# Optimization experiments

Measured on AMD Instinct MI355X. Metric: run time of the kernel, lower is better.

## Reference

```python
import jax, jax.numpy as jnp
import numpy as np

B, S, DIM, HEADS, FFN = 2, 2048, 2048, 16, 8192
HD = DIM // HEADS            # 128
F_, H_, W_ = 8, 16, 16       # F*H*W == S (video token grid)
CTX = 512
EPS = 1e-6


def _rope_tables(max_len=1024):
    # Wan-style rope_params: per-axis inverse-frequency tables, concatenated columns [22|21|21].
    c = HD // 2  # 64 complex channels
    splits = [c - 2 * (c // 3), c // 3, c // 3]
    pos = np.arange(max_len)[:, None].astype(np.float64)
    parts = []
    for d in splits:
        inv = 1.0 / (10000.0 ** (np.arange(d, dtype=np.float64) / d))
        parts.append(pos * inv[None, :])
    theta = np.concatenate(parts, axis=1)  # [max_len, 64]
    return (jnp.asarray(np.cos(theta), jnp.float32),
            jnp.asarray(np.sin(theta), jnp.float32))


def setup_inputs() -> dict:
    key = jax.random.key(0)
    ks = iter(jax.random.split(key, 40))
    def nrm(shape, scale=1.0):
        return jax.random.normal(next(ks), shape, jnp.float32) * scale
    ws = DIM ** -0.5
    cos, sin = _rope_tables()
    inp = dict(
        x=nrm((B, S, DIM)),
        e=nrm((B, 6, DIM)),
        context=nrm((B, CTX, DIM)),
        freqs_cos=cos, freqs_sin=sin,
        modulation=nrm((1, 6, DIM), ws),
        # self-attention (weights stored [in, out] so y = x @ W + b)
        sa_wq=nrm((DIM, DIM), ws), sa_bq=jnp.zeros((DIM,), jnp.float32),
        sa_wk=nrm((DIM, DIM), ws), sa_bk=jnp.zeros((DIM,), jnp.float32),
        sa_wv=nrm((DIM, DIM), ws), sa_bv=jnp.zeros((DIM,), jnp.float32),
        sa_wo=nrm((DIM, DIM), ws), sa_bo=jnp.zeros((DIM,), jnp.float32),
        sa_nq=jnp.ones((DIM,), jnp.float32), sa_nk=jnp.ones((DIM,), jnp.float32),
        # t2v cross-attention
        ca_wq=nrm((DIM, DIM), ws), ca_bq=jnp.zeros((DIM,), jnp.float32),
        ca_wk=nrm((DIM, DIM), ws), ca_bk=jnp.zeros((DIM,), jnp.float32),
        ca_wv=nrm((DIM, DIM), ws), ca_bv=jnp.zeros((DIM,), jnp.float32),
        ca_wo=nrm((DIM, DIM), ws), ca_bo=jnp.zeros((DIM,), jnp.float32),
        ca_nq=jnp.ones((DIM,), jnp.float32), ca_nk=jnp.ones((DIM,), jnp.float32),
        norm3_w=jnp.ones((DIM,), jnp.float32), norm3_b=jnp.zeros((DIM,), jnp.float32),
        ffn_w1=nrm((DIM, FFN), ws), ffn_b1=jnp.zeros((FFN,), jnp.float32),
        ffn_w2=nrm((FFN, DIM), FFN ** -0.5), ffn_b2=jnp.zeros((DIM,), jnp.float32),
    )
    return inp


def _ln(x, w=None, b=None, eps=EPS):
    m = jnp.mean(x, -1, keepdims=True)
    v = jnp.mean((x - m) ** 2, -1, keepdims=True)
    y = (x - m) * jax.lax.rsqrt(v + eps)
    return y * w + b if w is not None else y


def _rms(x, w, eps=EPS):
    return x * jax.lax.rsqrt(jnp.mean(x * x, -1, keepdims=True) + eps) * w


def _grid_cs(tab):
    # tab: [1024, 64] -> per-token table [S, 64] for grid (F_,H_,W_), split 22/21/21
    c = HD // 2
    s0 = c - 2 * (c // 3)  # 22
    s1 = c // 3            # 21
    f = jnp.broadcast_to(tab[:F_, :s0][:, None, None, :], (F_, H_, W_, s0))
    h = jnp.broadcast_to(tab[:H_, s0:s0 + s1][None, :, None, :], (F_, H_, W_, s1))
    w = jnp.broadcast_to(tab[:W_, s0 + s1:][None, None, :, :], (F_, H_, W_, s1))
    return jnp.concatenate([f, h, w], -1).reshape(S, c)


def _rope(x, cos, sin):
    # x: [B,S,N,D]; complex rotation on consecutive (even, odd) pairs
    xp = x.reshape(*x.shape[:-1], HD // 2, 2)
    xr, xi = xp[..., 0], xp[..., 1]
    c = cos[None, :, None, :]
    s = sin[None, :, None, :]
    return jnp.stack([xr * c - xi * s, xr * s + xi * c], -1).reshape(x.shape)


def _attn(q, k, v):
    logits = jnp.einsum('bqnd,bknd->bnqk', q, k) / np.float32(np.sqrt(HD))
    w = jax.nn.softmax(logits, axis=-1)
    return jnp.einsum('bnqk,bknd->bqnd', w, v)


def reference(x, e, context, freqs_cos, freqs_sin, modulation,
              sa_wq, sa_bq, sa_wk, sa_bk, sa_wv, sa_bv, sa_wo, sa_bo, sa_nq, sa_nk,
              ca_wq, ca_bq, ca_wk, ca_bk, ca_wv, ca_bv, ca_wo, ca_bo, ca_nq, ca_nk,
              norm3_w, norm3_b, ffn_w1, ffn_b1, ffn_w2, ffn_b2,
              seq_lens=None, grid_sizes=None, context_lens=None):
    # AdaLN modulation: 6 (shift, scale, gate) vectors per sample
    em = modulation + e                       # [B,6,D]
    e0, e1, e2, e3, e4, e5 = [em[:, i:i + 1, :] for i in range(6)]
    cos = _grid_cs(freqs_cos)
    sin = _grid_cs(freqs_sin)

    # --- self-attention with modulated LayerNorm + 3D RoPE ---
    xn = _ln(x) * (1 + e1) + e0
    q = _rms(xn @ sa_wq + sa_bq, sa_nq).reshape(B, S, HEADS, HD)
    k = _rms(xn @ sa_wk + sa_bk, sa_nk).reshape(B, S, HEADS, HD)
    v = (xn @ sa_wv + sa_bv).reshape(B, S, HEADS, HD)
    y = _attn(_rope(q, cos, sin), _rope(k, cos, sin), v).reshape(B, S, DIM)
    x = x + (y @ sa_wo + sa_bo) * e2

    # --- t2v cross-attention (affine norm3) ---
    xn3 = _ln(x, norm3_w, norm3_b)
    q = _rms(xn3 @ ca_wq + ca_bq, ca_nq).reshape(B, S, HEADS, HD)
    k = _rms(context @ ca_wk + ca_bk, ca_nk).reshape(B, CTX, HEADS, HD)
    v = (context @ ca_wv + ca_bv).reshape(B, CTX, HEADS, HD)
    y = _attn(q, k, v).reshape(B, S, DIM)
    x = x + (y @ ca_wo + ca_bo)

    # --- modulated FFN (GELU-tanh) ---
    xn2 = _ln(x) * (1 + e4) + e3
    y = jax.nn.gelu(xn2 @ ffn_w1 + ffn_b1, approximate=True) @ ffn_w2 + ffn_b2
    return x + y * e5
```

## Files before the change

### kernel.cpp

```cpp
#include <hip/hip_runtime.h>
#include <hip/hip_bf16.h>
#include <math.h>

#define DIMX 2048
#define SLEN 2048
#define BSZ 2
#define NHEADS 16
#define HDIM 128
#define FFND 8192
#define CTXL 512
#define LN_EPS 1e-6f

typedef __attribute__((ext_vector_type(8))) short short8_t;
typedef __attribute__((ext_vector_type(4))) short short4_t;
typedef __attribute__((ext_vector_type(4))) float f32x4;
typedef __hip_bfloat16 bf16;

__device__ __forceinline__ short f2bf(float f) {
  union { float f; unsigned u; } v; v.f = f;
  return (short)((v.u + 0x7FFFu + ((v.u >> 16) & 1u)) >> 16);
}
__device__ __forceinline__ float bf2f(short s) {
  union { unsigned u; float f; } v; v.u = ((unsigned)(unsigned short)s) << 16;
  return v.f;
}

__device__ __forceinline__ void gload16(const void* g, void* l) {
  __builtin_amdgcn_global_load_lds(
      (const __attribute__((address_space(1))) unsigned int*)g,
      (__attribute__((address_space(3))) unsigned int*)l, 16, 0, 0);
}

__device__ __forceinline__ float wred_sum(float v) {
#pragma unroll
  for (int o = 32; o > 0; o >>= 1) v += __shfl_xor(v, o, 64);
  return v;
}

__global__ void em_kernel(const float* __restrict__ e, const float* __restrict__ mod,
                          float* __restrict__ em, int n) {
  int i = blockIdx.x * 256 + threadIdx.x;
  if (i < n) em[i] = e[i] + mod[i % (6 * DIMX)];
}

__global__ void cvt_kernel(const float* __restrict__ in, bf16* __restrict__ out, int n8) {
  int i = blockIdx.x * 256 + threadIdx.x;
  if (i >= n8) return;
  float4 a = *(const float4*)(in + (size_t)i * 8);
  float4 b = *(const float4*)(in + (size_t)i * 8 + 4);
  float fv[8] = {a.x, a.y, a.z, a.w, b.x, b.y, b.z, b.w};
  short8_t o;
#pragma unroll
  for (int j = 0; j < 8; ++j) o[j] = f2bf(fv[j]);
  *(short8_t*)((short*)out + (size_t)i * 8) = o;
}

__global__ void packb_kernel(const float* b0, const float* b1, const float* b2,
                             float* __restrict__ dst, int n) {
  int i = blockIdx.x * 256 + threadIdx.x;
  if (i >= n) return;
  int seg = i >> 11, j = i & 2047;
  const float* s = seg == 0 ? b0 : (seg == 1 ? b1 : b2);
  dst[i] = s[j];
}

__global__ __launch_bounds__(256) void transpose_w(const float* __restrict__ W,
                                                   bf16* __restrict__ Wt, int K, int N,
                                                   int noff) {
  __shared__ short tile[64 * 68];
  int k0 = blockIdx.y << 6, n0 = blockIdx.x << 6;
  int t = threadIdx.x;
#pragma unroll
  for (int p = 0; p < 4; ++p) {
    int lin = p * 1024 + t * 4;
    int kr = lin >> 6, nc = lin & 63;
    float4 f = *(const float4*)(W + (size_t)(k0 + kr) * N + n0 + nc);
    tile[(nc + 0) * 68 + kr] = f2bf(f.x);
    tile[(nc + 1) * 68 + kr] = f2bf(f.y);
    tile[(nc + 2) * 68 + kr] = f2bf(f.z);
    tile[(nc + 3) * 68 + kr] = f2bf(f.w);
  }
  __syncthreads();
#pragma unroll
  for (int p = 0; p < 4; ++p) {
    int lin = p * 1024 + t * 4;
    int nr = lin >> 6, kc = lin & 63;
    short4_t s = *(const short4_t*)&tile[nr * 68 + kc];
    *(short4_t*)((short*)Wt + (size_t)(noff + n0 + nr) * K + k0 + kc) = s;
  }
}

__global__ __launch_bounds__(256) void ln_kernel(
    const float* __restrict__ x, const float* __restrict__ gamma,
    const float* __restrict__ beta, int gbstride, float addone,
    int rows_per_b, bf16* __restrict__ out) {
  int row = blockIdx.x;
  int t = threadIdx.x;
  const float* xr = x + (size_t)row * DIMX;
  float4 v0 = *(const float4*)(xr + t * 8);
  float4 v1 = *(const float4*)(xr + t * 8 + 4);
  float vv[8] = {v0.x, v0.y, v0.z, v0.w, v1.x, v1.y, v1.z, v1.w};
  float s = 0.f, ss = 0.f;
#pragma unroll
  for (int i = 0; i < 8; ++i) { s += vv[i]; ss += vv[i] * vv[i]; }
  __shared__ float red[8];
  s = wred_sum(s); ss = wred_sum(ss);
  int wid = t >> 6;
  if ((t & 63) == 0) { red[wid] = s; red[4 + wid] = ss; }
  __syncthreads();
  float sum = red[0] + red[1] + red[2] + red[3];
  float sumsq = red[4] + red[5] + red[6] + red[7];
  float mean = sum * (1.f / DIMX);
  float var = sumsq * (1.f / DIMX) - mean * mean;
  float rs = rsqrtf(var + LN_EPS);
  int b = row / rows_per_b;
  const float* g = gamma + (size_t)b * gbstride;
  const float* be = beta + (size_t)b * gbstride;
  short8_t o;
#pragma unroll
  for (int i = 0; i < 8; ++i) {
    int d = t * 8 + i;
    float y = (vv[i] - mean) * rs;
    o[i] = f2bf(y * (addone + g[d]) + be[d]);
  }
  *(short8_t*)((short*)out + (size_t)row * DIMX + t * 8) = o;
}

__global__ __launch_bounds__(256) void rms_rope_kernel(
    const bf16* __restrict__ x, int xstride, const float* __restrict__ w,
    const float* __restrict__ fcos, const float* __restrict__ fsin,
    int do_rope, bf16* __restrict__ out) {
  int row = blockIdx.x;
  int t = threadIdx.x;
  short8_t xi = *(const short8_t*)((const short*)x + (size_t)row * xstride + t * 8);
  float vv[8];
#pragma unroll
  for (int i = 0; i < 8; ++i) vv[i] = bf2f(xi[i]);
  float ss = 0.f;
#pragma unroll
  for (int i = 0; i < 8; ++i) ss += vv[i] * vv[i];
  __shared__ float red[4];
  ss = wred_sum(ss);
  int wid = t >> 6;
  if ((t & 63) == 0) red[wid] = ss;
  __syncthreads();
  float sumsq = red[0] + red[1] + red[2] + red[3];
  float rs = rsqrtf(sumsq * (1.f / DIMX) + LN_EPS);
  float y[8];
#pragma unroll
  for (int i = 0; i < 8; ++i) y[i] = vv[i] * rs * w[t * 8 + i];
  if (do_rope) {
    int s = row % SLEN;
    int f = s >> 8, hh = (s >> 4) & 15, ww = s & 15;
    int jb = ((t * 8) % HDIM) >> 1;
#pragma unroll
    for (int p = 0; p < 4; ++p) {
      int j = jb + p;
      int src = (j < 22) ? f : ((j < 43) ? hh : ww);
      float c = fcos[src * 64 + j];
      float sn = fsin[src * 64 + j];
      float xr_ = y[2 * p], xim = y[2 * p + 1];
      y[2 * p] = xr_ * c - xim * sn;
      y[2 * p + 1] = xr_ * sn + xim * c;
    }
  }
  short8_t o;
#pragma unroll
  for (int i = 0; i < 8; ++i) o[i] = f2bf(y[i]);
  *(short8_t*)((short*)out + (size_t)row * DIMX + t * 8) = o;
}

__global__ __launch_bounds__(256) void gemm_bt(
    const bf16* __restrict__ A, const bf16* __restrict__ Bt,
    const float* __restrict__ bias,
    float* outF, bf16* outB,
    const float* resid, const float* __restrict__ scale,
    int scstride, int rows_per_b, int gn, int N, int K, int mode) {
  __shared__ short As[2][128 * 64];
  __shared__ short Bs[2][128 * 64];
  int t = threadIdx.x, lane = t & 63, wv = t >> 6;
  int nwg = gridDim.x, cpx = nwg >> 3;
  int swz = (blockIdx.x & 7) * cpx + (blockIdx.x >> 3);
  int by = swz / gn, bx = swz % gn;
  int m0 = by << 7, n0 = bx << 7;
  f32x4 acc[4][4] = {};
  int mo_l = (wv >> 1) << 6, no_l = (wv & 1) << 6;

  int srow[4], scol[4];
#pragma unroll
  for (int j = 0; j < 4; ++j) {
    srow[j] = wv * 32 + j * 8 + (lane >> 3);
    scol[j] = ((lane & 7) ^ (srow[j] & 7)) << 3;
  }
  const short* Ap = (const short*)A;
  const short* Bp = (const short*)Bt;

  int koff = lane >> 4;
  int rowA[4], rowB[4];
#pragma unroll
  for (int i = 0; i < 4; ++i) {
    rowA[i] = mo_l + i * 16 + (lane & 15);
    rowB[i] = no_l + i * 16 + (lane & 15);
  }

  auto stage = [&](int buf, int kk) {
#pragma unroll
    for (int j = 0; j < 4; ++j) {
      gload16(Ap + (size_t)(m0 + srow[j]) * K + kk + scol[j],
              &As[buf][(wv * 32 + j * 8) * 64]);
      gload16(Bp + (size_t)(n0 + srow[j]) * K + kk + scol[j],
              &Bs[buf][(wv * 32 + j * 8) * 64]);
    }
  };

  stage(0, 0);
  __syncthreads();
  int cur = 0;
  for (int kk = 0; kk < K; kk += 64) {
    int nxt = cur ^ 1;
    if (kk + 64 < K) stage(nxt, kk + 64);
    short8_t af[2][4], bfv[2][4];
#pragma unroll
    for (int h = 0; h < 2; ++h)
#pragma unroll
      for (int i = 0; i < 4; ++i) {
        int cA = ((h * 4 + koff) ^ (rowA[i] & 7)) << 3;
        af[h][i] = *(const short8_t*)&As[cur][rowA[i] * 64 + cA];
        int cB = ((h * 4 + koff) ^ (rowB[i] & 7)) << 3;
        bfv[h][i] = *(const short8_t*)&Bs[cur][rowB[i] * 64 + cB];
      }
#pragma unroll
    for (int h = 0; h < 2; ++h)
#pragma unroll
      for (int mt = 0; mt < 4; ++mt)
#pragma unroll
        for (int nt = 0; nt < 4; ++nt)
          acc[mt][nt] = __builtin_amdgcn_mfma_f32_16x16x32_bf16(af[h][mt], bfv[h][nt], acc[mt][nt], 0, 0, 0);
    __syncthreads();
    cur = nxt;
  }

  int mo = m0 + mo_l, no = n0 + no_l;
#pragma unroll
  for (int mt = 0; mt < 4; ++mt)
#pragma unroll
    for (int nt = 0; nt < 4; ++nt) {
      int n = no + nt * 16 + (lane & 15);
      float bia = bias[n];
#pragma unroll
      for (int r = 0; r < 4; ++r) {
        int m = mo + mt * 16 + (lane >> 4) * 4 + r;
        float vv = acc[mt][nt][r] + bia;
        size_t idx = (size_t)m * N + n;
        if (mode == 1) {
          ((short*)outB)[idx] = f2bf(vv);
        } else if (mode == 2) {
          float g = 0.5f * vv * (1.f + tanhf(0.7978845608f * (vv + 0.044715f * vv * vv * vv)));
          ((short*)outB)[idx] = f2bf(g);
        } else {
          float sc = scale ? scale[(size_t)(m / rows_per_b) * scstride + n] : 1.0f;
          outF[idx] = resid[idx] + vv * sc;
        }
      }
    }
}

__global__ __launch_bounds__(256) void attn_kernel(
    const bf16* __restrict__ q, const bf16* __restrict__ k,
    const bf16* __restrict__ v, bf16* __restrict__ y,
    int QL, int KVL, int qs, int ks, int vs, float scl) {
  __shared__ short Kt[64 * 136];
  __shared__ short Vt[128 * 72];
  __shared__ short Pl[4 * 16 * 72];
  __shared__ float rl[4 * 16];
  __shared__ float ll[4 * 16];
  int t = threadIdx.x, lane = t & 63, wv = t >> 6;
  int bh = blockIdx.y;
  int b = bh / NHEADS, h = bh % NHEADS;
  int q0 = blockIdx.x * 64 + wv * 16;
  const short* qp = (const short*)q;
  const short* kp = (const short*)k;
  const short* vp = (const short*)v;
  short8_t qf[4];
  {
    size_t qbase = ((size_t)(b * QL) + q0 + (lane & 15)) * qs + h * HDIM + (lane >> 4) * 8;
#pragma unroll
    for (int kc = 0; kc < 4; ++kc) qf[kc] = *(const short8_t*)(qp + qbase + kc * 32);
  }
  f32x4 o[8] = {};
  float m_run = -1e30f, l_run = 0.f;
  int strow = t >> 2, stcol = (t & 3) * 32;
  for (int kt0 = 0; kt0 < KVL; kt0 += 64) {
    const short* ksrc = kp + ((size_t)(b * KVL + kt0 + strow) * ks + h * HDIM + stcol);
    const short* vsrc = vp + ((size_t)(b * KVL + kt0 + strow) * vs + h * HDIM + stcol);
#pragma unroll
    for (int c = 0; c < 4; ++c)
      *(short8_t*)&Kt[strow * 136 + stcol + c * 8] = *(const short8_t*)(ksrc + c * 8);
#pragma unroll
    for (int c = 0; c < 4; ++c) {
      short8_t vvv = *(const short8_t*)(vsrc + c * 8);
#pragma unroll
      for (int e = 0; e < 8; ++e) Vt[(stcol + c * 8 + e) * 72 + strow] = vvv[e];
    }
    __syncthreads();
    f32x4 st[4];
#pragma unroll
    for (int kt = 0; kt < 4; ++kt) {
      f32x4 a = {0.f, 0.f, 0.f, 0.f};
#pragma unroll
      for (int kc = 0; kc < 4; ++kc) {
        short8_t kf = *(const short8_t*)&Kt[(kt * 16 + (lane & 15)) * 136 + kc * 32 + (lane >> 4) * 8];
        a = __builtin_amdgcn_mfma_f32_16x16x32_bf16(kf, qf[kc], a, 0, 0, 0);
      }
      st[kt] = a;
    }
    float mt_ = -1e30f;
#pragma unroll
    for (int kt = 0; kt < 4; ++kt)
#pragma unroll
      for (int r = 0; r < 4; ++r) mt_ = fmaxf(mt_, st[kt][r]);
    mt_ = fmaxf(mt_, __shfl_xor(mt_, 16, 64));
    mt_ = fmaxf(mt_, __shfl_xor(mt_, 32, 64));
    mt_ *= scl;
    float m_new = fmaxf(m_run, mt_);
    float rfac = __expf(m_run - m_new);
    float ps = 0.f;
#pragma unroll
    for (int kt = 0; kt < 4; ++kt)
#pragma unroll
      for (int r = 0; r < 4; ++r) {
        float p = __expf(st[kt][r] * scl - m_new);
        st[kt][r] = p;
        ps += p;
      }
    ps += __shfl_xor(ps, 16, 64);
    ps += __shfl_xor(ps, 32, 64);
    l_run = l_run * rfac + ps;
    m_run = m_new;
    if (lane < 16) rl[wv * 16 + lane] = rfac;
#pragma unroll
    for (int kt = 0; kt < 4; ++kt)
#pragma unroll
      for (int r = 0; r < 4; ++r)
        Pl[(wv * 16 + (lane & 15)) * 72 + kt * 16 + (lane >> 4) * 4 + r] = f2bf(st[kt][r]);
    float rr[4];
#pragma unroll
    for (int r = 0; r < 4; ++r) rr[r] = rl[wv * 16 + (lane >> 4) * 4 + r];
#pragma unroll
    for (int dt = 0; dt < 8; ++dt)
#pragma unroll
      for (int r = 0; r < 4; ++r) o[dt][r] *= rr[r];
#pragma unroll
    for (int kc2 = 0; kc2 < 2; ++kc2) {
      short8_t pa = *(const short8_t*)&Pl[(wv * 16 + (lane & 15)) * 72 + kc2 * 32 + (lane >> 4) * 8];
#pragma unroll
      for (int dt = 0; dt < 8; ++dt) {
        short8_t vf = *(const short8_t*)&Vt[(dt * 16 + (lane & 15)) * 72 + kc2 * 32 + (lane >> 4) * 8];
        o[dt] = __builtin_amdgcn_mfma_f32_16x16x32_bf16(pa, vf, o[dt], 0, 0, 0);
      }
    }
    __syncthreads();
  }
  if (lane < 16) ll[wv * 16 + lane] = 1.f / l_run;
  float li[4];
#pragma unroll
  for (int r = 0; r < 4; ++r) li[r] = ll[wv * 16 + (lane >> 4) * 4 + r];
  short* yp = (short*)y;
#pragma unroll
  for (int dt = 0; dt < 8; ++dt)
#pragma unroll
    for (int r = 0; r < 4; ++r) {
      int qq = q0 + (lane >> 4) * 4 + r;
      int d = dt * 16 + (lane & 15);
      yp[((size_t)(b * QL) + qq) * DIMX + h * HDIM + d] = f2bf(o[dt][r] * li[r]);
    }
}

#define OFF_EM    0ull
#define OFF_BQKV  (512ull << 10)
#define OFF_BCKV  (560ull << 10)
#define OFF_XN    (1ull << 20)
#define OFF_QKV   (17ull << 20)
#define OFF_CAQ   (17ull << 20)
#define OFF_KV    (33ull << 20)
#define OFF_QB    (65ull << 20)
#define OFF_KB    (81ull << 20)
#define OFF_YB    (97ull << 20)
#define OFF_CTX   (113ull << 20)
#define OFF_WBUF  (117ull << 20)
#define OFF_HB    (17ull << 20)

extern "C" void kernel_launch(void* const* d_in, const int* in_sizes, int n_in,
                              void* d_out, int out_size, void* d_ws, size_t ws_size,
                              hipStream_t stream) {
  const float* x       = (const float*)d_in[0];
  const float* e       = (const float*)d_in[1];
  const float* context = (const float*)d_in[2];
  const float* fcos    = (const float*)d_in[3];
  const float* fsin    = (const float*)d_in[4];
  const float* modu    = (const float*)d_in[5];
  const float* sa_wq = (const float*)d_in[6];  const float* sa_bq = (const float*)d_in[7];
  const float* sa_wk = (const float*)d_in[8];  const float* sa_bk = (const float*)d_in[9];
  const float* sa_wv = (const float*)d_in[10]; const float* sa_bv = (const float*)d_in[11];
  const float* sa_wo = (const float*)d_in[12]; const float* sa_bo = (const float*)d_in[13];
  const float* sa_nq = (const float*)d_in[14]; const float* sa_nk = (const float*)d_in[15];
  const float* ca_wq = (const float*)d_in[16]; const float* ca_bq = (const float*)d_in[17];
  const float* ca_wk = (const float*)d_in[18]; const float* ca_bk = (const float*)d_in[19];
  const float* ca_wv = (const float*)d_in[20]; const float* ca_bv = (const float*)d_in[21];
  const float* ca_wo = (const float*)d_in[22]; const float* ca_bo = (const float*)d_in[23];
  const float* ca_nq = (const float*)d_in[24]; const float* ca_nk = (const float*)d_in[25];
  const float* n3_w  = (const float*)d_in[26]; const float* n3_b  = (const float*)d_in[27];
  const float* f_w1  = (const float*)d_in[28]; const float* f_b1  = (const float*)d_in[29];
  const float* f_w2  = (const float*)d_in[30]; const float* f_b2  = (const float*)d_in[31];

  char* ws = (char*)d_ws;
  float* em   = (float*)(ws + OFF_EM);
  float* bqkv = (float*)(ws + OFF_BQKV);
  float* bckv = (float*)(ws + OFF_BCKV);
  bf16* xn    = (bf16*)(ws + OFF_XN);
  bf16* qkvb  = (bf16*)(ws + OFF_QKV);
  bf16* caqb  = (bf16*)(ws + OFF_CAQ);
  bf16* kvb   = (bf16*)(ws + OFF_KV);
  bf16* qb    = (bf16*)(ws + OFF_QB);
  bf16* kb    = (bf16*)(ws + OFF_KB);
  bf16* yb    = (bf16*)(ws + OFF_YB);
  bf16* ctxb  = (bf16*)(ws + OFF_CTX);
  bf16* wbuf  = (bf16*)(ws + OFF_WBUF);
  bf16* hb    = (bf16*)(ws + OFF_HB);
  float* xw   = (float*)d_out;

  const int M = BSZ * SLEN;
  const int MC = BSZ * CTXL;
  const float scl = 0.08838834764831845f;

#define TRANSO(W, Kd, Nd, noff) \
  transpose_w<<<dim3((Nd) / 64, (Kd) / 64), 256, 0, stream>>>(W, wbuf, Kd, Nd, noff)
#define GEMM(Am, Md, Nd, Kd, bias, oF, oB, res, sc, scs, rpb, mode) \
  gemm_bt<<<((Md) / 128) * ((Nd) / 128), 256, 0, stream>>>(Am, wbuf, bias, oF, oB, res, sc, scs, rpb, (Nd) / 128, Nd, Kd, mode)

  em_kernel<<<(BSZ * 6 * DIMX + 255) / 256, 256, 0, stream>>>(e, modu, em, BSZ * 6 * DIMX);
  cvt_kernel<<<(MC * DIMX / 8 + 255) / 256, 256, 0, stream>>>(context, ctxb, MC * DIMX / 8);
  packb_kernel<<<(3 * DIMX + 255) / 256, 256, 0, stream>>>(sa_bq, sa_bk, sa_bv, bqkv, 3 * DIMX);
  packb_kernel<<<(2 * DIMX + 255) / 256, 256, 0, stream>>>(ca_bk, ca_bv, nullptr, bckv, 2 * DIMX);

  ln_kernel<<<M, 256, 0, stream>>>(x, em + 1 * DIMX, em + 0 * DIMX, 6 * DIMX, 1.0f, SLEN, xn);

  TRANSO(sa_wq, DIMX, DIMX, 0);
  TRANSO(sa_wk, DIMX, DIMX, DIMX);
  TRANSO(sa_wv, DIMX, DIMX, 2 * DIMX);
  GEMM(xn, M, 3 * DIMX, DIMX, bqkv, nullptr, qkvb, nullptr, nullptr, 0, 1, 1);
  rms_rope_kernel<<<M, 256, 0, stream>>>(qkvb, 3 * DIMX, sa_nq, fcos, fsin, 1, qb);
  rms_rope_kernel<<<M, 256, 0, stream>>>((bf16*)((short*)qkvb + DIMX), 3 * DIMX, sa_nk, fcos, fsin, 1, kb);

  attn_kernel<<<dim3(SLEN / 64, BSZ * NHEADS), 256, 0, stream>>>(
      qb, kb, (bf16*)((short*)qkvb + 2 * DIMX), yb, SLEN, SLEN, DIMX, DIMX, 3 * DIMX, scl);

  TRANSO(sa_wo, DIMX, DIMX, 0);
  GEMM(yb, M, DIMX, DIMX, sa_bo, xw, nullptr, x, em + 2 * DIMX, 6 * DIMX, SLEN, 3);

  ln_kernel<<<M, 256, 0, stream>>>(xw, n3_w, n3_b, 0, 0.0f, SLEN, xn);

  TRANSO(ca_wq, DIMX, DIMX, 0);
  GEMM(xn, M, DIMX, DIMX, ca_bq, nullptr, caqb, nullptr, nullptr, 0, 1, 1);
  rms_rope_kernel<<<M, 256, 0, stream>>>(caqb, DIMX, ca_nq, fcos, fsin, 0, qb);

  TRANSO(ca_wk, DIMX, DIMX, 0);
  TRANSO(ca_wv, DIMX, DIMX, DIMX);
  GEMM(ctxb, MC, 2 * DIMX, DIMX, bckv, nullptr, kvb, nullptr, nullptr, 0, 1, 1);
  rms_rope_kernel<<<MC, 256, 0, stream>>>(kvb, 2 * DIMX, ca_nk, fcos, fsin, 0, kb);

  attn_kernel<<<dim3(SLEN / 64, BSZ * NHEADS), 256, 0, stream>>>(
      qb, kb, (bf16*)((short*)kvb + DIMX), yb, SLEN, CTXL, DIMX, DIMX, 2 * DIMX, scl);

  TRANSO(ca_wo, DIMX, DIMX, 0);
  GEMM(yb, M, DIMX, DIMX, ca_bo, xw, nullptr, xw, nullptr, 0, SLEN, 3);

  ln_kernel<<<M, 256, 0, stream>>>(xw, em + 4 * DIMX, em + 3 * DIMX, 6 * DIMX, 1.0f, SLEN, xn);

  TRANSO(f_w1, DIMX, FFND, 0);
  GEMM(xn, M, FFND, DIMX, f_b1, nullptr, hb, nullptr, nullptr, 0, 1, 2);

  TRANSO(f_w2, FFND, DIMX, 0);
  GEMM(hb, M, DIMX, FFND, f_b2, xw, nullptr, xw, em + 5 * DIMX, 6 * DIMX, SLEN, 3);
}
```

Measured before the change: 1.120 ms.

## Add 256x256-tile 8-wave GEMM with ping-pong scheduling and split-K FFN2

```diff
diff --git a/kernel.cpp b/kernel.cpp
--- a/kernel.cpp
+++ b/kernel.cpp
@@ -170,6 +170,124 @@
   *(short8_t*)((short*)out + (size_t)row * DIMX + t * 8) = o;
 }
 
+#define RD_A(mh) { _Pragma("unroll") for (int mi = 0; mi < 4; ++mi) { \
+    int r = wm * 128 + (mh) * 64 + mi * 16 + l15; int rb = r * 64; int r7 = r & 7; \
+    a[mi][0] = *(const short8_t*)&As[buf][rb + ((koff ^ r7) << 3)]; \
+    a[mi][1] = *(const short8_t*)&As[buf][rb + (((4 + koff) ^ r7) << 3)]; } }
+#define RD_B(nh) { _Pragma("unroll") for (int nj = 0; nj < 2; ++nj) { \
+    int r = wn * 64 + (nh) * 32 + nj * 16 + l15; int rb = r * 64; int r7 = r & 7; \
+    b[nj][0] = *(const short8_t*)&Bs[buf][rb + ((koff ^ r7) << 3)]; \
+    b[nj][1] = *(const short8_t*)&Bs[buf][rb + (((4 + koff) ^ r7) << 3)]; } }
+#define MMA(mh, nh) { _Pragma("unroll") for (int kk = 0; kk < 2; ++kk) \
+    _Pragma("unroll") for (int mi = 0; mi < 4; ++mi) \
+    _Pragma("unroll") for (int nj = 0; nj < 2; ++nj) \
+      acc[(mh)*4+mi][(nh)*2+nj] = __builtin_amdgcn_mfma_f32_16x16x32_bf16( \
+          a[mi][kk], b[nj][kk], acc[(mh)*4+mi][(nh)*2+nj], 0, 0, 0); }
+#define BAR asm volatile("s_barrier" ::: "memory")
+#define SETPRIO(x) __builtin_amdgcn_s_setprio(x)
+
+__global__ __launch_bounds__(512) void gemm256(
+    const bf16* __restrict__ A, const bf16* __restrict__ Bt,
+    const float* __restrict__ bias,
+    float* outF, bf16* outB,
+    const float* resid, const float* __restrict__ scale, const float* part,
+    int scstride, int rows_per_b, int gn, int N, int K, int lda, int ldb,
+    int k0, int mode) {
+  __shared__ short As[2][16384];
+  __shared__ short Bs[2][16384];
+  int t = threadIdx.x, lane = t & 63, wv = t >> 6;
+  int l15 = lane & 15, koff = lane >> 4;
+  int wm = wv >> 2, wn = wv & 3;
+  int nwg = gridDim.x, cpx = nwg >> 3;
+  int swz = (blockIdx.x & 7) * cpx + (blockIdx.x >> 3);
+  int by = swz / gn, bx = swz % gn;
+  int m0 = by << 8, n0 = bx << 8;
+
+  f32x4 acc[8][4] = {};
+  short8_t a[4][2], b[2][2];
+
+  int srcChunk = ((lane & 7) ^ (lane >> 3)) << 3;
+  int rowInSlot = lane >> 3;
+  const short* Ap = (const short*)A;
+  const short* Bp = (const short*)Bt;
+
+  auto stageA = [&](int bufI, int kkE, int late) {
+#pragma unroll
+    for (int i = 0; i < 2; ++i) {
+      int idx = i * 8 + wv;
+      int slot = ((idx >> 3) << 4) + (idx & 7) + (late ? 8 : 0);
+      int row = slot * 8 + rowInSlot;
+      gload16(Ap + (size_t)(m0 + row) * lda + kkE + srcChunk, &As[bufI][slot << 9]);
+    }
+  };
+  auto stageB = [&](int bufI, int kkE, int late) {
+#pragma unroll
+    for (int i = 0; i < 2; ++i) {
+      int idx = i * 8 + wv;
+      int slot = ((idx >> 2) << 3) + (idx & 3) + (late ? 4 : 0);
+      int row = slot * 8 + rowInSlot;
+      gload16(Bp + (size_t)(n0 + row) * ldb + kkE + srcChunk, &Bs[bufI][slot << 9]);
+    }
+  };
+
+  int NT = K >> 6;
+  stageA(0, k0, 0); stageB(0, k0, 0);
+  stageA(0, k0, 1); stageB(0, k0, 1);
+  stageA(1, k0 + 64, 0); stageB(1, k0 + 64, 0);
+  asm volatile("s_waitcnt vmcnt(4)" ::: "memory");
+  BAR;
+
+  for (int tt = 0; tt < NT; ++tt) {
+    int buf = tt & 1;
+    int kk1 = k0 + (((tt + 1) < NT ? (tt + 1) : 0) << 6);
+    int kk2 = k0 + (((tt + 2) < NT ? (tt + 2) : 0) << 6);
+    RD_A(0); RD_B(0);
+    stageA(buf ^ 1, kk1, 1);
+    BAR; SETPRIO(1); MMA(0, 0); SETPRIO(0); BAR;
+    RD_B(1);
+    stageB(buf ^ 1, kk1, 1);
+    BAR; SETPRIO(1); MMA(0, 1); SETPRIO(0); BAR;
+    RD_A(1); RD_B(0);
+    stageA(buf, kk2, 0);
+    BAR; SETPRIO(1); MMA(1, 0); SETPRIO(0); BAR;
+    RD_B(1);
+    stageB(buf, kk2, 0);
+    BAR; SETPRIO(1); MMA(1, 1); SETPRIO(0);
+    asm volatile("s_waitcnt vmcnt(4)" ::: "memory");
+    BAR;
+  }
+  asm volatile("s_waitcnt vmcnt(0)" ::: "memory");
+
+  int mo = m0 + wm * 128, no = n0 + wn * 64;
+#pragma unroll
+  for (int mf = 0; mf < 8; ++mf)
+#pragma unroll
+    for (int nf = 0; nf < 4; ++nf) {
+      int n = no + nf * 16 + l15;
+      float bia = (mode == 0) ? 0.f : bias[n];
+#pragma unroll
+      for (int r = 0; r < 4; ++r) {
+        int m = mo + mf * 16 + koff * 4 + r;
+        float vv = acc[mf][nf][r] + bia;
+        size_t idx = (size_t)m * N + n;
+        if (mode == 0) {
+          outF[idx] = vv;
+        } else if (mode == 1) {
+          ((short*)outB)[idx] = f2bf(vv);
+        } else if (mode == 2) {
+          float g = 0.5f * vv * (1.f + tanhf(0.7978845608f * (vv + 0.044715f * vv * vv * vv)));
+          ((short*)outB)[idx] = f2bf(g);
+        } else if (mode == 3) {
+          float sc = scale ? scale[(size_t)(m / rows_per_b) * scstride + n] : 1.0f;
+          outF[idx] = resid[idx] + vv * sc;
+        } else {
+          float sc = scale ? scale[(size_t)(m / rows_per_b) * scstride + n] : 1.0f;
+          outF[idx] = resid[idx] + (part[idx] + vv) * sc;
+        }
+      }
+    }
+}
+
 __global__ __launch_bounds__(256) void gemm_bt(
     const bf16* __restrict__ A, const bf16* __restrict__ Bt,
     const float* __restrict__ bias,
@@ -203,13 +321,13 @@
     rowB[i] = no_l + i * 16 + (lane & 15);
   }
 
-  auto stage = [&](int buf, int kk) {
+  auto stage = [&](int bufI, int kk) {
 #pragma unroll
     for (int j = 0; j < 4; ++j) {
       gload16(Ap + (size_t)(m0 + srow[j]) * K + kk + scol[j],
-              &As[buf][(wv * 32 + j * 8) * 64]);
+              &As[bufI][(wv * 32 + j * 8) * 64]);
       gload16(Bp + (size_t)(n0 + srow[j]) * K + kk + scol[j],
-              &Bs[buf][(wv * 32 + j * 8) * 64]);
+              &Bs[bufI][(wv * 32 + j * 8) * 64]);
     }
   };
 
@@ -306,13 +424,13 @@
     f32x4 st[4];
 #pragma unroll
     for (int kt = 0; kt < 4; ++kt) {
-      f32x4 a = {0.f, 0.f, 0.f, 0.f};
+      f32x4 aa = {0.f, 0.f, 0.f, 0.f};
 #pragma unroll
       for (int kc = 0; kc < 4; ++kc) {
         short8_t kf = *(const short8_t*)&Kt[(kt * 16 + (lane & 15)) * 136 + kc * 32 + (lane >> 4) * 8];
-        a = __builtin_amdgcn_mfma_f32_16x16x32_bf16(kf, qf[kc], a, 0, 0, 0);
+        aa = __builtin_amdgcn_mfma_f32_16x16x32_bf16(kf, qf[kc], aa, 0, 0, 0);
       }
-      st[kt] = a;
+      st[kt] = aa;
     }
     float mt_ = -1e30f;
 #pragma unroll
@@ -389,6 +507,7 @@
 #define OFF_CTX   (113ull << 20)
 #define OFF_WBUF  (117ull << 20)
 #define OFF_HB    (17ull << 20)
+#define OFF_P0    (81ull << 20)
 
 extern "C" void kernel_launch(void* const* d_in, const int* in_sizes, int n_in,
                               void* d_out, int out_size, void* d_ws, size_t ws_size,
@@ -427,6 +546,7 @@
   bf16* ctxb  = (bf16*)(ws + OFF_CTX);
   bf16* wbuf  = (bf16*)(ws + OFF_WBUF);
   bf16* hb    = (bf16*)(ws + OFF_HB);
+  float* p0   = (float*)(ws + OFF_P0);
   float* xw   = (float*)d_out;
 
   const int M = BSZ * SLEN;
@@ -435,7 +555,10 @@
 
 #define TRANSO(W, Kd, Nd, noff) \
   transpose_w<<<dim3((Nd) / 64, (Kd) / 64), 256, 0, stream>>>(W, wbuf, Kd, Nd, noff)
-#define GEMM(Am, Md, Nd, Kd, bias, oF, oB, res, sc, scs, rpb, mode) \
+#define GEMM256(Am, Md, Nd, Kd, ldA, ldB, kOff, bias, oF, oB, res, sc, prt, scs, rpb, mode) \
+  gemm256<<<((Md) / 256) * ((Nd) / 256), 512, 0, stream>>>(Am, wbuf, bias, oF, oB, res, sc, prt, \
+                                                           scs, rpb, (Nd) / 256, Nd, Kd, ldA, ldB, kOff, mode)
+#define GEMM128(Am, Md, Nd, Kd, bias, oF, oB, res, sc, scs, rpb, mode) \
   gemm_bt<<<((Md) / 128) * ((Nd) / 128), 256, 0, stream>>>(Am, wbuf, bias, oF, oB, res, sc, scs, rpb, (Nd) / 128, Nd, Kd, mode)
 
   em_kernel<<<(BSZ * 6 * DIMX + 255) / 256, 256, 0, stream>>>(e, modu, em, BSZ * 6 * DIMX);
@@ -448,7 +571,8 @@
   TRANSO(sa_wq, DIMX, DIMX, 0);
   TRANSO(sa_wk, DIMX, DIMX, DIMX);
   TRANSO(sa_wv, DIMX, DIMX, 2 * DIMX);
-  GEMM(xn, M, 3 * DIMX, DIMX, bqkv, nullptr, qkvb, nullptr, nullptr, 0, 1, 1);
+  GEMM256(xn, M, 3 * DIMX, DIMX, DIMX, DIMX, 0, bqkv, nullptr, qkvb,
+          nullptr, nullptr, nullptr, 0, 1, 1);
   rms_rope_kernel<<<M, 256, 0, stream>>>(qkvb, 3 * DIMX, sa_nq, fcos, fsin, 1, qb);
   rms_rope_kernel<<<M, 256, 0, stream>>>((bf16*)((short*)qkvb + DIMX), 3 * DIMX, sa_nk, fcos, fsin, 1, kb);
 
@@ -456,30 +580,37 @@
       qb, kb, (bf16*)((short*)qkvb + 2 * DIMX), yb, SLEN, SLEN, DIMX, DIMX, 3 * DIMX, scl);
 
   TRANSO(sa_wo, DIMX, DIMX, 0);
-  GEMM(yb, M, DIMX, DIMX, sa_bo, xw, nullptr, x, em + 2 * DIMX, 6 * DIMX, SLEN, 3);
+  GEMM256(yb, M, DIMX, DIMX, DIMX, DIMX, 0, sa_bo, xw, nullptr,
+          x, em + 2 * DIMX, nullptr, 6 * DIMX, SLEN, 3);
 
   ln_kernel<<<M, 256, 0, stream>>>(xw, n3_w, n3_b, 0, 0.0f, SLEN, xn);
 
   TRANSO(ca_wq, DIMX, DIMX, 0);
-  GEMM(xn, M, DIMX, DIMX, ca_bq, nullptr, caqb, nullptr, nullptr, 0, 1, 1);
+  GEMM256(xn, M, DIMX, DIMX, DIMX, DIMX, 0, ca_bq, nullptr, caqb,
+          nullptr, nullptr, nullptr, 0, 1, 1);
   rms_rope_kernel<<<M, 256, 0, stream>>>(caqb, DIMX, ca_nq, fcos, fsin, 0, qb);
 
   TRANSO(ca_wk, DIMX, DIMX, 0);
   TRANSO(ca_wv, DIMX, DIMX, DIMX);
-  GEMM(ctxb, MC, 2 * DIMX, DIMX, bckv, nullptr, kvb, nullptr, nullptr, 0, 1, 1);
+  GEMM128(ctxb, MC, 2 * DIMX, DIMX, bckv, nullptr, kvb, nullptr, nullptr, 0, 1, 1);
   rms_rope_kernel<<<MC, 256, 0, stream>>>(kvb, 2 * DIMX, ca_nk, fcos, fsin, 0, kb);
 
   attn_kernel<<<dim3(SLEN / 64, BSZ * NHEADS), 256, 0, stream>>>(
       qb, kb, (bf16*)((short*)kvb + DIMX), yb, SLEN, CTXL, DIMX, DIMX, 2 * DIMX, scl);
 
   TRANSO(ca_wo, DIMX, DIMX, 0);
-  GEMM(yb, M, DIMX, DIMX, ca_bo, xw, nullptr, xw, nullptr, 0, SLEN, 3);
+  GEMM256(yb, M, DIMX, DIMX, DIMX, DIMX, 0, ca_bo, xw, nullptr,
+          xw, nullptr, nullptr, 0, SLEN, 3);
 
   ln_kernel<<<M, 256, 0, stream>>>(xw, em + 4 * DIMX, em + 3 * DIMX, 6 * DIMX, 1.0f, SLEN, xn);
 
   TRANSO(f_w1, DIMX, FFND, 0);
-  GEMM(xn, M, FFND, DIMX, f_b1, nullptr, hb, nullptr, nullptr, 0, 1, 2);
+  GEMM256(xn, M, FFND, DIMX, DIMX, DIMX, 0, f_b1, nullptr, hb,
+          nullptr, nullptr, nullptr, 0, 1, 2);
 
   TRANSO(f_w2, FFND, DIMX, 0);
-  GEMM(hb, M, DIMX, FFND, f_b2, xw, nullptr, xw, em + 5 * DIMX, 6 * DIMX, SLEN, 3);
-}
+  GEMM256(hb, M, DIMX, FFND / 2, FFND, FFND, 0, f_b2, p0, nullptr,
+          nullptr, nullptr, nullptr, 0, 1, 0);
+  GEMM256(hb, M, DIMX, FFND / 2, FFND, FFND, FFND / 2, f_b2, xw, nullptr,
+          xw, em + 5 * DIMX, p0, 6 * DIMX, SLEN, 4);
+}
```

Result: slower. 1.374 ms (+22.7%).
